# Kernel optimization log

Measured on AMD Instinct MI355X. Metric: run time of the kernel, lower is better.

Reference implementation:

```python
import jax, jax.numpy as jnp
import numpy as np

N_NODES = 100000
NEG_SLOPE = 0.01  # F.leaky_relu default


def leaky_relu(x):
    return jnp.where(x >= 0, x, NEG_SLOPE * x)


def setup_inputs() -> dict:
    key = jax.random.key(0)
    ks = jax.random.split(key, 8)
    F_in, H, E, B = 256, 64, 1600000, 16384
    x = jax.random.normal(ks[0], (N_NODES, F_in), dtype=jnp.float32)
    edge_index = jax.random.randint(ks[1], (2, E), 0, N_NODES, dtype=jnp.int64)
    index = jax.random.randint(ks[2], (B, 2), 0, N_NODES, dtype=jnp.int64)
    W_conv = jax.random.normal(ks[3], (F_in, H), dtype=jnp.float32) / np.sqrt(F_in)
    b_conv = jnp.zeros((H,), dtype=jnp.float32)
    W1 = jax.random.normal(ks[4], (2 * H, 16), dtype=jnp.float32) / np.sqrt(2 * H)
    b1 = jnp.zeros((16,), dtype=jnp.float32)
    W2 = jax.random.normal(ks[5], (16, 1), dtype=jnp.float32) / np.sqrt(16)
    b2 = jnp.zeros((1,), dtype=jnp.float32)
    return {"x": x, "edge_index": edge_index, "index": index,
            "W_conv": W_conv, "b_conv": b_conv,
            "W1": W1, "b1": b1, "W2": W2, "b2": b2}


def reference(x, edge_index, index, W_conv, b_conv, W1, b1, W2, b2):
    N = x.shape[0]
    # --- GCNConv: linear transform, add self-loops, symmetric normalization, scatter-add ---
    h = x @ W_conv                                   # [N, H]
    loops = jnp.arange(N, dtype=edge_index.dtype)
    src = jnp.concatenate([edge_index[0], loops])    # [E+N]
    dst = jnp.concatenate([edge_index[1], loops])    # [E+N]
    deg = jax.ops.segment_sum(jnp.ones_like(dst, dtype=h.dtype), dst, num_segments=N)
    dinv = jnp.where(deg > 0, jax.lax.rsqrt(deg), 0.0)
    norm = dinv[src] * dinv[dst]                     # [E+N]
    msg = h[src] * norm[:, None]                     # [E+N, H]
    node_embed = jax.ops.segment_sum(msg, dst, num_segments=N) + b_conv
    # dropout is a no-op in eval mode; then leaky_relu
    node_embed = leaky_relu(node_embed)
    # --- edge-pair gather + MLP head ---
    x_i = node_embed[index[:, 0]]                    # [B, H]
    x_j = node_embed[index[:, 1]]                    # [B, H]
    out = jnp.concatenate([x_i, x_j], axis=1)        # [B, 2H]
    out = leaky_relu(out @ W1 + b1)                  # [B, 16]
    out = out @ W2 + b2                              # [B, 1]
    return jax.nn.sigmoid(out)
```

## Files before the change

### kernel.cpp

```cpp
#include <hip/hip_runtime.h>
#include <hip/hip_bf16.h>

#define NN 100000
#define FIN 256
#define FH 64
#define NEG 0.01f
#define NBUCK 256
#define BNODES ((NN + NBUCK - 1) / NBUCK)
#define P1_CH 4096
#define WP 264
#define SRCMASK 0x1FFFF
#define SLAB 16384
#define GA 782
#define GB 781

typedef __attribute__((ext_vector_type(8))) short short8x;
typedef __attribute__((ext_vector_type(4))) float f32x4;

__device__ inline unsigned short f2bf_hw(float f) {
    __hip_bfloat16 h = __float2bfloat16(f);
    return __builtin_bit_cast(unsigned short, h);
}
__device__ inline float bf2f(unsigned short s) {
    return __uint_as_float(((unsigned)s) << 16);
}

__device__ inline long long load_idx(const void* p, long long i, int is64) {
    if (is64) return ((const long long*)p)[i];
    return (long long)((const int*)p)[i];
}

__device__ inline int is64_ballot(const void* p) {
    const int* p32 = (const int*)p;
    int lane = threadIdx.x & 63;
    int ok = (p32[2 * lane + 1] == 0) ? 1 : 0;
    unsigned long long m = __ballot(ok);
    return m == ~0ULL ? 1 : 0;
}


__global__ __launch_bounds__(256) void prep_kernel(int* __restrict__ coarse_cursor,
                                                   unsigned char* __restrict__ flags) {
    const int b = blockIdx.x, t = threadIdx.x;
    if (b == 0) {
        coarse_cursor[t] = t * SLAB;
    } else {
        int i = (b - 1) * 256 + t;
        if (i < NN) flags[i] = 0;
    }
}

__device__ void gemm_role(const float* __restrict__ x, const float* __restrict__ W,
                          unsigned short* __restrict__ hbf, int gb, char* smem) {
    unsigned short* Wt = (unsigned short*)smem;

    for (int i = threadIdx.x; i < FIN * FH; i += 256) {
        int k = i >> 6, c = i & 63;
        Wt[c * WP + k] = f2bf_hw(W[i]);
    }
    __syncthreads();

    const int wv = threadIdx.x >> 6;
    const int lane = threadIdx.x & 63;
    const int c = lane & 15;
    const int eg = lane >> 4;

    const int row0 = (gb * 4 + wv) * 16;
    int rowA = row0 + c;
    if (rowA >= NN) rowA = NN - 1;
    const float* aptr = x + (long long)rowA * FIN;

    f32x4 acc[4] = {{0,0,0,0},{0,0,0,0},{0,0,0,0},{0,0,0,0}};

#pragma unroll
    for (int kk = 0; kk < 8; ++kk) {
        const int kbase = kk * 32 + eg * 8;
        float4 f0 = *(const float4*)(aptr + kbase);
        float4 f1 = *(const float4*)(aptr + kbase + 4);
        short8x a;
        a[0] = (short)f2bf_hw(f0.x); a[1] = (short)f2bf_hw(f0.y);
        a[2] = (short)f2bf_hw(f0.z); a[3] = (short)f2bf_hw(f0.w);
        a[4] = (short)f2bf_hw(f1.x); a[5] = (short)f2bf_hw(f1.y);
        a[6] = (short)f2bf_hw(f1.z); a[7] = (short)f2bf_hw(f1.w);
#pragma unroll
        for (int cb = 0; cb < 4; ++cb) {
            short8x b = *(const short8x*)(&Wt[(cb * 16 + c) * WP + kbase]);
            acc[cb] = __builtin_amdgcn_mfma_f32_16x16x32_bf16(a, b, acc[cb], 0, 0, 0);
        }
    }

#pragma unroll
    for (int cb = 0; cb < 4; ++cb) {
#pragma unroll
        for (int r = 0; r < 4; ++r) {
            int rowO = row0 + eg * 4 + r;
            if (rowO < NN)
                hbf[(long long)rowO * FH + cb * 16 + c] = f2bf_hw(acc[cb][r]);
        }
    }
}

__device__ void part_role(const void* __restrict__ ei, int* __restrict__ coarse_cursor,
                          int* __restrict__ pairs, int E, int pb, char* smem) {
    int* hist = (int*)smem;
    int* blkoff = hist + NBUCK;
    const int t = threadIdx.x;
    hist[t] = 0;
    __syncthreads();
    const int is64 = is64_ballot(ei);
    const long long base = (long long)pb * P1_CH;

    int pkv[16], bkt[16], rnk[16];
#pragma unroll
    for (int i = 0; i < 16; ++i) {
        long long e = base + i * 256 + t;
        if (e < E) {
            int s = (int)load_idx(ei, e, is64);
            int d = (int)load_idx(ei, (long long)E + e, is64);
            int b = (int)((unsigned)d / BNODES);
            int dl = d - b * BNODES;
            pkv[i] = s | (dl << 17);
            bkt[i] = b;
            rnk[i] = atomicAdd(&hist[b], 1);
        } else {
            bkt[i] = -1;
        }
    }
    __syncthreads();
    blkoff[t] = atomicAdd(&coarse_cursor[t], hist[t]);
    __syncthreads();
#pragma unroll
    for (int i = 0; i < 16; ++i) {
        if (bkt[i] >= 0) {
            int pos = blkoff[bkt[i]] + rnk[i];
            if (pos < (bkt[i] + 1) * SLAB)
                pairs[pos] = pkv[i];
        }
    }
}

__device__ void mark_role(const void* __restrict__ idx, unsigned char* __restrict__ flags,
                          int nIdx, int mb) {
    const int is64 = is64_ballot(idx);
    int i = mb * 256 + threadIdx.x;
    if (i < nIdx) flags[load_idx(idx, i, is64)] = 1;
}

__device__ void place_role(const int* __restrict__ pairs,
                           const int* __restrict__ coarse_cursor,
                           int* __restrict__ cursor, float* __restrict__ dinv,
                           int* __restrict__ bucket,
                           const unsigned char* __restrict__ flags,
                           int b, char* smem) {
    int* cnt = (int*)smem;
    int* nstart = cnt + BNODES;
    int* wsum = nstart + BNODES + 1;
    int* sh = wsum + 8;
    unsigned char* nflag = (unsigned char*)(sh + 2);
    const int t = threadIdx.x;
    const int lane = t & 63, w = t >> 6;

    int myc = coarse_cursor[t] - t * SLAB;
    if (myc > SLAB) myc = SLAB;
    int incl0 = myc;
#pragma unroll
    for (int m = 1; m < 64; m <<= 1) {
        int u = __shfl_up(incl0, m, 64);
        if (lane >= m) incl0 += u;
    }
    if (lane == 63) wsum[w] = incl0;
    __syncthreads();
    int woff0 = 0;
    for (int i = 0; i < w; ++i) woff0 += wsum[i];
    int ex0 = woff0 + incl0 - myc;
    if (t == b) { sh[0] = ex0; sh[1] = myc; }
    __syncthreads();
    const int lo = sh[0];
    const int cntb = sh[1];
    const int g0 = b * BNODES;
    const int nb = (NN - g0 < BNODES) ? (NN - g0) : BNODES;
    const int sb = b * SLAB;

    for (int j = t; j < nb; j += 256) {
        cnt[j] = 0;
        nflag[j] = flags[g0 + j];
    }
    __syncthreads();

    for (int i = t; i < cntb; i += 256)
        atomicAdd(&cnt[pairs[sb + i] >> 17], 1);
    __syncthreads();

    const int i0 = 2 * t, i1 = 2 * t + 1;
    const int v0 = (i0 < nb) ? cnt[i0] : 0;
    const int v1 = (i1 < nb) ? cnt[i1] : 0;
    const int s = v0 + v1;
    int incl = s;
#pragma unroll
    for (int m = 1; m < 64; m <<= 1) {
        int u = __shfl_up(incl, m, 64);
        if (lane >= m) incl += u;
    }
    __syncthreads();
    if (lane == 63) wsum[w] = incl;
    __syncthreads();
    int woff = 0;
    for (int i = 0; i < w; ++i) woff += wsum[i];
    const int ex = woff + incl - s;
    if (i0 <= nb) nstart[i0] = ex;
    if (i1 <= nb) nstart[i1] = ex + v0;
    __syncthreads();

    for (int j = t; j <= nb; j += 256) {
        int g = g0 + j;
        if (g <= NN) cursor[g] = lo + nstart[j];
    }
    for (int j = t; j < nb; j += 256)
        dinv[g0 + j] = rsqrtf(1.0f + (float)(nstart[j + 1] - nstart[j]));

    for (int j = t; j < nb; j += 256) cnt[j] = 0;
    __syncthreads();
    for (int i = t; i < cntb; i += 256) {
        int p = pairs[sb + i];
        int local = p >> 17;
        if (nflag[local]) {
            int r = atomicAdd(&cnt[local], 1);
            bucket[lo + nstart[local] + r] = p & SRCMASK;
        }
    }
}

__global__ __launch_bounds__(256) void fusedA_kernel(const float* __restrict__ x,
                                                     const float* __restrict__ W,
                                                     unsigned short* __restrict__ hbf,
                                                     const void* __restrict__ ei,
                                                     int* __restrict__ coarse_cursor,
                                                     int* __restrict__ pairs, int E,
                                                     const void* __restrict__ idx,
                                                     unsigned char* __restrict__ flags,
                                                     int nIdx, int npart) {
    __shared__ __align__(16) char smem[FH * WP * 2];
    const int b = blockIdx.x;
    if (b < GA)              gemm_role(x, W, hbf, b, smem);
    else if (b < GA + npart) part_role(ei, coarse_cursor, pairs, E, b - GA, smem);
    else                     mark_role(idx, flags, nIdx, b - GA - npart);
}

__global__ __launch_bounds__(256) void fusedB_kernel(const float* __restrict__ x,
                                                     const float* __restrict__ W,
                                                     unsigned short* __restrict__ hbf,
                                                     const int* __restrict__ pairs,
                                                     const int* __restrict__ coarse_cursor,
                                                     int* __restrict__ cursor,
                                                     float* __restrict__ dinv,
                                                     int* __restrict__ bucket,
                                                     const unsigned char* __restrict__ flags) {
    __shared__ __align__(16) char smem[FH * WP * 2];
    const int b = blockIdx.x;
    if (b < GB) gemm_role(x, W, hbf, GA + b, smem);
    else        place_role(pairs, coarse_cursor, cursor, dinv, bucket, flags, b - GB, smem);
}

__global__ __launch_bounds__(256) void gather8_kernel(const unsigned short* __restrict__ hbf,
                                                      const float* __restrict__ dinv,
                                                      const int* __restrict__ cursor,
                                                      const int* __restrict__ bucket,
                                                      const float* __restrict__ b_conv,
                                                      const unsigned char* __restrict__ flags,
                                                      float* __restrict__ ne) {
    const int node = blockIdx.x * 4 + (threadIdx.x >> 6);
    if (node >= NN) return;
    if (!flags[node]) return;
    const int lane = threadIdx.x & 63;
    const int sub = lane & 7;
    const int eg = lane >> 3;

    const int base = cursor[node];
    const int end  = cursor[node + 1];
    const float dd = dinv[node];

    float acc[8] = {0,0,0,0,0,0,0,0};
    for (int k = base + eg; k < end; k += 8) {
        int s = bucket[k];
        float nrm = dinv[s] * dd;
        short8x hv = *(const short8x*)(hbf + (long long)s * FH + sub * 8);
#pragma unroll
        for (int j = 0; j < 8; ++j)
            acc[j] += bf2f((unsigned short)hv[j]) * nrm;
    }
#pragma unroll
    for (int m = 8; m < 64; m <<= 1) {
#pragma unroll
        for (int j = 0; j < 8; ++j) acc[j] += __shfl_xor(acc[j], m);
    }
    if (eg == 0) {
        short8x hs = *(const short8x*)(hbf + (long long)node * FH + sub * 8);
        float r[8];
#pragma unroll
        for (int j = 0; j < 8; ++j) {
            float v = acc[j] + bf2f((unsigned short)hs[j]) * dd * dd + b_conv[sub * 8 + j];
            r[j] = v >= 0.f ? v : NEG * v;
        }
        float4* o = (float4*)(ne + (long long)node * FH + sub * 8);
        o[0] = make_float4(r[0], r[1], r[2], r[3]);
        o[1] = make_float4(r[4], r[5], r[6], r[7]);
    }
}

__global__ __launch_bounds__(256) void mlp_kernel(const float* __restrict__ ne,
                                                  const void* __restrict__ idx,
                                                  const float* __restrict__ W1,
                                                  const float* __restrict__ b1,
                                                  const float* __restrict__ W2,
                                                  const float* __restrict__ b2,
                                                  float* __restrict__ out,
                                                  int B) {
    const int lane = threadIdx.x & 63;
    const int wid = threadIdx.x >> 6;
    const int is64 = is64_ballot(idx);

    float w1a[16], w1b[16], b1r[16], w2r[16];
#pragma unroll
    for (int o = 0; o < 16; ++o) {
        w1a[o] = W1[lane * 16 + o];
        w1b[o] = W1[(64 + lane) * 16 + o];
        b1r[o] = b1[o];
        w2r[o] = W2[o];
    }
    const float b2v = b2[0];

    for (int pair = blockIdx.x * 4 + wid; pair < B; pair += gridDim.x * 4) {
        long long i0 = load_idx(idx, 2LL * pair, is64);
        long long i1 = load_idx(idx, 2LL * pair + 1, is64);
        float a = ne[i0 * FH + lane];
        float b = ne[i1 * FH + lane];

        float acc[16];
#pragma unroll
        for (int o = 0; o < 16; ++o) acc[o] = a * w1a[o] + b * w1b[o];
#pragma unroll
        for (int m = 1; m < 64; m <<= 1) {
#pragma unroll
            for (int o = 0; o < 16; ++o) acc[o] += __shfl_xor(acc[o], m, 64);
        }
        if (lane == 0) {
            float s = b2v;
#pragma unroll
            for (int o = 0; o < 16; ++o) {
                float z = acc[o] + b1r[o];
                z = z >= 0.f ? z : NEG * z;
                s += z * w2r[o];
            }
            out[pair] = 1.f / (1.f + expf(-s));
        }
    }
}


__global__ void detect_kernel(const int* __restrict__ ei32, int* __restrict__ flag) {
    if (blockIdx.x == 0 && threadIdx.x == 0) {
        int ok = 1;
        for (int k = 0; k < 64; ++k)
            if (ei32[2 * k + 1] != 0) { ok = 0; break; }
        *flag = ok;
    }
}

__global__ __launch_bounds__(256) void gemm_kernel(const float* __restrict__ x,
                                                   const float* __restrict__ W,
                                                   float* __restrict__ h) {
    __shared__ float xs[4 * FIN];
    __shared__ float part[4][4][FH];

    const int col = threadIdx.x & 63;
    const int kseg = threadIdx.x >> 6;

    float wreg[64];
#pragma unroll
    for (int kk = 0; kk < 64; ++kk)
        wreg[kk] = W[(kseg * 64 + kk) * FH + col];

    for (int row0 = blockIdx.x * 4; row0 < NN; row0 += gridDim.x * 4) {
        const float4* xv = (const float4*)(x + (long long)row0 * FIN);
        ((float4*)xs)[threadIdx.x] = xv[threadIdx.x];
        __syncthreads();

        float acc[4] = {0.f, 0.f, 0.f, 0.f};
#pragma unroll
        for (int kk = 0; kk < 64; ++kk) {
            const float w = wreg[kk];
            const int k = kseg * 64 + kk;
#pragma unroll
            for (int r = 0; r < 4; ++r)
                acc[r] += xs[r * FIN + k] * w;
        }
#pragma unroll
        for (int r = 0; r < 4; ++r) part[r][kseg][col] = acc[r];
        __syncthreads();

        const int row = threadIdx.x >> 6;
        float s = part[row][0][col] + part[row][1][col] + part[row][2][col] + part[row][3][col];
        h[(long long)(row0 + row) * FH + col] = s;
        __syncthreads();
    }
}

__global__ __launch_bounds__(256) void init_kernel(float* __restrict__ ne,
                                                   float* __restrict__ deg,
                                                   const float* __restrict__ b_conv) {
    int idx = blockIdx.x * 256 + threadIdx.x;
    if (idx < NN * FH) ne[idx] = b_conv[idx & (FH - 1)];
    if (idx < NN) deg[idx] = 1.0f;
}

__global__ __launch_bounds__(256) void deg_kernel(const void* __restrict__ ei,
                                                  float* __restrict__ deg,
                                                  int E, const int* __restrict__ flag) {
    int e = blockIdx.x * 256 + threadIdx.x;
    if (e >= E) return;
    long long d = load_idx(ei, (long long)E + e, *flag);
    atomicAdd(&deg[d], 1.0f);
}

__global__ __launch_bounds__(256) void rsqrt_kernel(float* __restrict__ deg) {
    int i = blockIdx.x * 256 + threadIdx.x;
    if (i < NN) deg[i] = rsqrtf(deg[i]);
}

__global__ __launch_bounds__(256) void selfloop_kernel(const float* __restrict__ h,
                                                       const float* __restrict__ dinv,
                                                       float* __restrict__ ne) {
    int idx = blockIdx.x * 256 + threadIdx.x;
    if (idx >= NN * FH) return;
    int i = idx >> 6;
    float di = dinv[i];
    ne[idx] += h[idx] * di * di;
}

__global__ __launch_bounds__(256) void edge_agg_kernel(const void* __restrict__ ei,
                                                       const float* __restrict__ dinv,
                                                       const float* __restrict__ h,
                                                       float* __restrict__ ne,
                                                       int E, const int* __restrict__ flag) {
    long long t = (long long)blockIdx.x * 256 + threadIdx.x;
    long long e = t >> 4;
    int sub = (int)(t & 15);
    if (e >= E) return;
    int is64 = *flag;
    long long s = load_idx(ei, e, is64);
    long long d = load_idx(ei, (long long)E + e, is64);
    float nrm = dinv[s] * dinv[d];
    float4 hv = *(const float4*)(h + s * FH + sub * 4);
    float* np_ = ne + d * FH + sub * 4;
    atomicAdd(np_ + 0, hv.x * nrm);
    atomicAdd(np_ + 1, hv.y * nrm);
    atomicAdd(np_ + 2, hv.z * nrm);
    atomicAdd(np_ + 3, hv.w * nrm);
}

__global__ __launch_bounds__(256) void mlp_fb_kernel(const float* __restrict__ ne,
                                                     const void* __restrict__ idx,
                                                     const float* __restrict__ W1,
                                                     const float* __restrict__ b1,
                                                     const float* __restrict__ W2,
                                                     const float* __restrict__ b2,
                                                     float* __restrict__ out,
                                                     int B, const int* __restrict__ flag) {
    const int lane = threadIdx.x & 63;
    const int wid = threadIdx.x >> 6;

    float w1a[16], w1b[16], b1r[16], w2r[16];
#pragma unroll
    for (int o = 0; o < 16; ++o) {
        w1a[o] = W1[lane * 16 + o];
        w1b[o] = W1[(64 + lane) * 16 + o];
        b1r[o] = b1[o];
        w2r[o] = W2[o];
    }
    const float b2v = b2[0];
    const int is64 = *flag;

    for (int pair = blockIdx.x * 4 + wid; pair < B; pair += gridDim.x * 4) {
        long long i0 = load_idx(idx, 2LL * pair, is64);
        long long i1 = load_idx(idx, 2LL * pair + 1, is64);
        float a = ne[i0 * FH + lane];
        float b = ne[i1 * FH + lane];
        a = a >= 0.f ? a : NEG * a;
        b = b >= 0.f ? b : NEG * b;

        float acc[16];
#pragma unroll
        for (int o = 0; o < 16; ++o) acc[o] = a * w1a[o] + b * w1b[o];
#pragma unroll
        for (int m = 1; m < 64; m <<= 1) {
#pragma unroll
            for (int o = 0; o < 16; ++o) acc[o] += __shfl_xor(acc[o], m, 64);
        }
        if (lane == 0) {
            float s = b2v;
#pragma unroll
            for (int o = 0; o < 16; ++o) {
                float z = acc[o] + b1r[o];
                z = z >= 0.f ? z : NEG * z;
                s += z * w2r[o];
            }
            out[pair] = 1.f / (1.f + expf(-s));
        }
    }
}

extern "C" void kernel_launch(void* const* d_in, const int* in_sizes, int n_in,
                              void* d_out, int out_size, void* d_ws, size_t ws_size,
                              hipStream_t stream) {
    const float* x      = (const float*)d_in[0];
    const void*  ei     = d_in[1];
    const void*  index  = d_in[2];
    const float* W_conv = (const float*)d_in[3];
    const float* b_conv = (const float*)d_in[4];
    const float* W1     = (const float*)d_in[5];
    const float* b1     = (const float*)d_in[6];
    const float* W2     = (const float*)d_in[7];
    const float* b2     = (const float*)d_in[8];
    float* out = (float*)d_out;

    const int E = in_sizes[1] / 2;
    const int B = in_sizes[2] / 2;

    const size_t need_new = (size_t)NN * FH * 2
                          + ((size_t)NN * FH + NN + (NN + 1) + (size_t)E + NBUCK) * 4
                          + NN;

    if (ws_size >= need_new && (size_t)NBUCK * SLAB <= (size_t)NN * FH) {
        unsigned short* hbf = (unsigned short*)d_ws;
        float* ne       = (float*)(hbf + (long long)NN * FH);
        float* dinv     = ne + (long long)NN * FH;
        int*   cursor   = (int*)(dinv + NN);
        int*   bucket   = cursor + (NN + 1);
        int*   coarse_cursor = bucket + E;
        unsigned char* flags = (unsigned char*)(coarse_cursor + NBUCK);
        int*   pairs    = (int*)ne;

        const int npart = (E + P1_CH - 1) / P1_CH;
        const int nmark = (2 * B + 255) / 256;

        prep_kernel<<<1 + (NN + 255) / 256, 256, 0, stream>>>(coarse_cursor, flags);
        fusedA_kernel<<<GA + npart + nmark, 256, 0, stream>>>(x, W_conv, hbf, ei,
                                                              coarse_cursor, pairs, E,
                                                              index, flags, 2 * B, npart);
        fusedB_kernel<<<GB + NBUCK, 256, 0, stream>>>(x, W_conv, hbf, pairs, coarse_cursor,
                                                      cursor, dinv, bucket, flags);
        gather8_kernel<<<(NN + 3) / 4, 256, 0, stream>>>(hbf, dinv, cursor, bucket,
                                                         b_conv, flags, ne);
        mlp_kernel<<<512, 256, 0, stream>>>(ne, index, W1, b1, W2, b2, out, B);
    } else {
        float* h   = (float*)d_ws;
        float* ne  = h + (long long)NN * FH;
        float* deg = ne + (long long)NN * FH;
        int* flag  = (int*)(deg + NN);

        detect_kernel<<<1, 64, 0, stream>>>((const int*)ei, flag);
        init_kernel<<<(NN * FH + 255) / 256, 256, 0, stream>>>(ne, deg, b_conv);
        gemm_kernel<<<2048, 256, 0, stream>>>(x, W_conv, h);
        deg_kernel<<<(E + 255) / 256, 256, 0, stream>>>(ei, deg, E, flag);
        rsqrt_kernel<<<(NN + 255) / 256, 256, 0, stream>>>(deg);
        selfloop_kernel<<<(NN * FH + 255) / 256, 256, 0, stream>>>(h, deg, ne);
        edge_agg_kernel<<<(int)(((long long)E * 16 + 255) / 256), 256, 0, stream>>>(ei, deg, h, ne, E, flag);
        mlp_fb_kernel<<<512, 256, 0, stream>>>(ne, index, W1, b1, W2, b2, out, B, flag);
    }
}
```

Baseline: 119.9 us.

## Fuse neighbor aggregation into MLP head, computing embeddings per query pair

Drops the separate gather kernel over all flagged nodes and the fp32 node-embedding buffer. Each wavefront now handles one query pair: its two halves aggregate the neighbors of the two endpoint nodes, then lanes are reshuffled into the existing MLP layout. This removes one launch and the round trip of embeddings through global memory. In exchange, a node appearing in several pairs is aggregated more than once, and each node gets only 4 edge slots instead of 8.

New measurement: 104.0 us, median of 2. 13.3% less time.

```diff
diff --git a/kernel.cpp b/kernel.cpp
--- a/kernel.cpp
+++ b/kernel.cpp
@@ -261,62 +261,23 @@
     else        place_role(pairs, coarse_cursor, cursor, dinv, bucket, flags, b - GB, smem);
 }
 
-__global__ __launch_bounds__(256) void gather8_kernel(const unsigned short* __restrict__ hbf,
-                                                      const float* __restrict__ dinv,
-                                                      const int* __restrict__ cursor,
-                                                      const int* __restrict__ bucket,
-                                                      const float* __restrict__ b_conv,
-                                                      const unsigned char* __restrict__ flags,
-                                                      float* __restrict__ ne) {
-    const int node = blockIdx.x * 4 + (threadIdx.x >> 6);
-    if (node >= NN) return;
-    if (!flags[node]) return;
+__global__ __launch_bounds__(256) void gmlp_kernel(const unsigned short* __restrict__ hbf,
+                                                   const float* __restrict__ dinv,
+                                                   const int* __restrict__ cursor,
+                                                   const int* __restrict__ bucket,
+                                                   const float* __restrict__ b_conv,
+                                                   const void* __restrict__ idx,
+                                                   const float* __restrict__ W1,
+                                                   const float* __restrict__ b1,
+                                                   const float* __restrict__ W2,
+                                                   const float* __restrict__ b2,
+                                                   float* __restrict__ out,
+                                                   int B) {
+    const int pair = blockIdx.x * 4 + (threadIdx.x >> 6);
     const int lane = threadIdx.x & 63;
-    const int sub = lane & 7;
-    const int eg = lane >> 3;
-
-    const int base = cursor[node];
-    const int end  = cursor[node + 1];
-    const float dd = dinv[node];
-
-    float acc[8] = {0,0,0,0,0,0,0,0};
-    for (int k = base + eg; k < end; k += 8) {
-        int s = bucket[k];
-        float nrm = dinv[s] * dd;
-        short8x hv = *(const short8x*)(hbf + (long long)s * FH + sub * 8);
-#pragma unroll
-        for (int j = 0; j < 8; ++j)
-            acc[j] += bf2f((unsigned short)hv[j]) * nrm;
-    }
-#pragma unroll
-    for (int m = 8; m < 64; m <<= 1) {
-#pragma unroll
-        for (int j = 0; j < 8; ++j) acc[j] += __shfl_xor(acc[j], m);
-    }
-    if (eg == 0) {
-        short8x hs = *(const short8x*)(hbf + (long long)node * FH + sub * 8);
-        float r[8];
-#pragma unroll
-        for (int j = 0; j < 8; ++j) {
-            float v = acc[j] + bf2f((unsigned short)hs[j]) * dd * dd + b_conv[sub * 8 + j];
-            r[j] = v >= 0.f ? v : NEG * v;
-        }
-        float4* o = (float4*)(ne + (long long)node * FH + sub * 8);
-        o[0] = make_float4(r[0], r[1], r[2], r[3]);
-        o[1] = make_float4(r[4], r[5], r[6], r[7]);
-    }
-}
-
-__global__ __launch_bounds__(256) void mlp_kernel(const float* __restrict__ ne,
-                                                  const void* __restrict__ idx,
-                                                  const float* __restrict__ W1,
-                                                  const float* __restrict__ b1,
-                                                  const float* __restrict__ W2,
-                                                  const float* __restrict__ b2,
-                                                  float* __restrict__ out,
-                                                  int B) {
-    const int lane = threadIdx.x & 63;
-    const int wid = threadIdx.x >> 6;
+    const int sub  = lane & 7;
+    const int slot = (lane >> 3) & 3;
+    const int half = lane >> 5;
     const int is64 = is64_ballot(idx);
 
     float w1a[16], w1b[16], b1r[16], w2r[16];
@@ -328,31 +289,63 @@
         w2r[o] = W2[o];
     }
     const float b2v = b2[0];
-
-    for (int pair = blockIdx.x * 4 + wid; pair < B; pair += gridDim.x * 4) {
-        long long i0 = load_idx(idx, 2LL * pair, is64);
-        long long i1 = load_idx(idx, 2LL * pair + 1, is64);
-        float a = ne[i0 * FH + lane];
-        float b = ne[i1 * FH + lane];
-
-        float acc[16];
-#pragma unroll
-        for (int o = 0; o < 16; ++o) acc[o] = a * w1a[o] + b * w1b[o];
-#pragma unroll
-        for (int m = 1; m < 64; m <<= 1) {
-#pragma unroll
-            for (int o = 0; o < 16; ++o) acc[o] += __shfl_xor(acc[o], m, 64);
-        }
-        if (lane == 0) {
-            float s = b2v;
-#pragma unroll
-            for (int o = 0; o < 16; ++o) {
-                float z = acc[o] + b1r[o];
-                z = z >= 0.f ? z : NEG * z;
-                s += z * w2r[o];
-            }
-            out[pair] = 1.f / (1.f + expf(-s));
-        }
+    if (pair >= B) return;
+
+    const long long i0 = load_idx(idx, 2LL * pair, is64);
+    const long long i1 = load_idx(idx, 2LL * pair + 1, is64);
+    const long long node = half ? i1 : i0;
+
+    const int base = cursor[node];
+    const int end  = cursor[node + 1];
+    const float dd = dinv[node];
+
+    float acc[8] = {0,0,0,0,0,0,0,0};
+    for (int k = base + slot; k < end; k += 4) {
+        int s = bucket[k];
+        float nrm = dinv[s] * dd;
+        short8x hv = *(const short8x*)(hbf + (long long)s * FH + sub * 8);
+#pragma unroll
+        for (int j = 0; j < 8; ++j)
+            acc[j] += bf2f((unsigned short)hv[j]) * nrm;
+    }
+#pragma unroll
+    for (int m = 8; m <= 16; m <<= 1) {
+#pragma unroll
+        for (int j = 0; j < 8; ++j) acc[j] += __shfl_xor(acc[j], m);
+    }
+    short8x hs = *(const short8x*)(hbf + (long long)node * FH + sub * 8);
+    float val[8];
+#pragma unroll
+    for (int j = 0; j < 8; ++j) {
+        float v = acc[j] + bf2f((unsigned short)hs[j]) * dd * dd + b_conv[sub * 8 + j];
+        val[j] = v >= 0.f ? v : NEG * v;
+    }
+
+    float a = 0.f, b = 0.f;
+#pragma unroll
+    for (int q = 0; q < 8; ++q) {
+        float va = __shfl(val[q], lane >> 3);
+        float vb = __shfl(val[q], 32 + (lane >> 3));
+        if ((lane & 7) == q) { a = va; b = vb; }
+    }
+
+    float acc16[16];
+#pragma unroll
+    for (int o = 0; o < 16; ++o) acc16[o] = a * w1a[o] + b * w1b[o];
+#pragma unroll
+    for (int m = 1; m < 64; m <<= 1) {
+#pragma unroll
+        for (int o = 0; o < 16; ++o) acc16[o] += __shfl_xor(acc16[o], m, 64);
+    }
+    if (lane == 0) {
+        float s = b2v;
+#pragma unroll
+        for (int o = 0; o < 16; ++o) {
+            float z = acc16[o] + b1r[o];
+            z = z >= 0.f ? z : NEG * z;
+            s += z * w2r[o];
+        }
+        out[pair] = 1.f / (1.f + expf(-s));
     }
 }
 
@@ -532,13 +525,13 @@
 
     if (ws_size >= need_new && (size_t)NBUCK * SLAB <= (size_t)NN * FH) {
         unsigned short* hbf = (unsigned short*)d_ws;
-        float* ne       = (float*)(hbf + (long long)NN * FH);
-        float* dinv     = ne + (long long)NN * FH;
+        float* scratch  = (float*)(hbf + (long long)NN * FH);
+        float* dinv     = scratch + (long long)NN * FH;
         int*   cursor   = (int*)(dinv + NN);
         int*   bucket   = cursor + (NN + 1);
         int*   coarse_cursor = bucket + E;
         unsigned char* flags = (unsigned char*)(coarse_cursor + NBUCK);
-        int*   pairs    = (int*)ne;
+        int*   pairs    = (int*)scratch;
 
         const int npart = (E + P1_CH - 1) / P1_CH;
         const int nmark = (2 * B + 255) / 256;
@@ -549,9 +542,8 @@
                                                               index, flags, 2 * B, npart);
         fusedB_kernel<<<GB + NBUCK, 256, 0, stream>>>(x, W_conv, hbf, pairs, coarse_cursor,
                                                       cursor, dinv, bucket, flags);
-        gather8_kernel<<<(NN + 3) / 4, 256, 0, stream>>>(hbf, dinv, cursor, bucket,
-                                                         b_conv, flags, ne);
-        mlp_kernel<<<512, 256, 0, stream>>>(ne, index, W1, b1, W2, b2, out, B);
+        gmlp_kernel<<<(B + 3) / 4, 256, 0, stream>>>(hbf, dinv, cursor, bucket, b_conv,
+                                                     index, W1, b1, W2, b2, out, B);
     } else {
         float* h   = (float*)d_ws;
         float* ne  = h + (long long)NN * FH;
```
